# Kernel optimization log

Hardware: AMD Instinct MI355X
Metric: run time of the kernel (lower is better)

The kernel has to match this reference:

```python
import jax, jax.numpy as jnp
import numpy as np
import math

FACTOR = 5  # module default

def setup_inputs() -> dict:
    key = jax.random.key(0)
    kq, kk, kv, ki = jax.random.split(key, 4)
    B, L, S, H, D = 2, 4096, 4096, 8, 64
    u_part = min(FACTOR * math.ceil(math.log(L)), S)  # 45: sampled keys per query
    return {
        "queries": jax.random.normal(kq, (B, L, H, D), jnp.float32),
        "keys": jax.random.normal(kk, (B, S, H, D), jnp.float32),
        "values": jax.random.normal(kv, (B, S, H, D), jnp.float32),
        "index_sample": jax.random.randint(ki, (L, u_part), 0, S),
    }

def reference(queries, keys, values, index_sample):
    # queries: [B,L,H,D], keys/values: [B,S,H,D], index_sample: [L,u_part]
    B, L, H, D = queries.shape
    S = keys.shape[1]
    Q = jnp.transpose(queries, (0, 2, 1, 3))  # [B,H,L,D]
    K = jnp.transpose(keys, (0, 2, 1, 3))     # [B,H,S,D]
    V = jnp.transpose(values, (0, 2, 1, 3))   # [B,H,S,D]
    U_part = min(FACTOR * math.ceil(math.log(S)), L)  # n_top queries (static)

    # --- _prob_QK: sample keys, sparsity measure M, top-k queries ---
    K_sample = K[:, :, index_sample, :]  # gather -> [B,H,L,u_part,D]
    QK_sample = jnp.einsum('bhld,bhlud->bhlu', Q, K_sample)  # [B,H,L,u_part]
    M = QK_sample.max(axis=-1) - QK_sample.sum(axis=-1) / S  # [B,H,L]
    _, M_top = jax.lax.top_k(M, U_part)                      # [B,H,U_part]
    Q_reduce = jnp.take_along_axis(Q, M_top[..., None], axis=2)  # [B,H,U_part,D]
    scores = jnp.einsum('bhud,bhsd->bhus', Q_reduce, K)          # [B,H,U_part,S]

    # --- mask_flag=False branch: plain scaled softmax attention ---
    scale = 1.0 / math.sqrt(D)
    attn = jax.nn.softmax(scores * scale, axis=-1)  # [B,H,U_part,S]
    context = jnp.einsum('bhus,bhsd->bhud', attn, V)  # [B,H,U_part,D]
    return context, attn
```

## Files before the change

kernel.cpp:

```cpp
#include <hip/hip_runtime.h>

#define BB 2
#define LL 4096
#define SS 4096
#define HH 8
#define DD 64
#define UU 45
#define SCALE 0.125f
#define NCH 32
#define CHK 128

__global__ __launch_bounds__(256) void k_compute_M(
    const float* __restrict__ q, const float* __restrict__ k,
    const int* __restrict__ idx, float* __restrict__ M) {
  __shared__ int sidx[16 * UU];
  int tid = threadIdx.x;
  int bh = blockIdx.x & 15;
  int l0 = (blockIdx.x >> 4) << 4;
  for (int i = tid; i < 16 * UU; i += 256) sidx[i] = idx[(long)l0 * UU + i];
  __syncthreads();

  int slot = tid >> 4;
  int sub  = tid & 15;
  int l = l0 + slot;
  int b = bh >> 3, h = bh & 7;

  const float4* qp = (const float4*)(q + (((long)b * LL + l) * HH + h) * DD);
  float4 qq = qp[sub];
  const float* kb = k + (long)b * SS * HH * DD + h * DD;

  float mx = -INFINITY, sm = 0.f;
  #pragma unroll 5
  for (int u = 0; u < UU; ++u) {
    int s = sidx[slot * UU + u];
    float4 kk4 = ((const float4*)(kb + (long)s * (HH * DD)))[sub];
    float p = qq.x * kk4.x + qq.y * kk4.y + qq.z * kk4.z + qq.w * kk4.w;
    #pragma unroll
    for (int off = 8; off; off >>= 1) p += __shfl_xor(p, off, 16);
    mx = fmaxf(mx, p);
    sm += p;
  }
  if (sub == 0) M[(long)bh * LL + l] = mx - sm * (1.0f / SS);
}

__global__ __launch_bounds__(256) void k_topk(
    const float* __restrict__ M, int* __restrict__ Mtop) {
  __shared__ unsigned keys[LL];
  __shared__ int hist[256];
  __shared__ int wsum[4];
  __shared__ int sh_bin, sh_gtwin;
  __shared__ int ccount, ecount;
  __shared__ unsigned cand_key[64];
  __shared__ int cand_idx[64];
  __shared__ int elist[LL];

  int bh = blockIdx.x, tid = threadIdx.x;
  int lane = tid & 63, w = tid >> 6;
  const float* m = M + (long)bh * LL;
  for (int i = tid; i < LL; i += 256) {
    union { float f; unsigned u; } cv; cv.f = m[i];
    keys[i] = (cv.u & 0x80000000u) ? ~cv.u : (cv.u | 0x80000000u);
  }
  if (tid == 0) { ccount = 0; ecount = 0; }
  __syncthreads();

  unsigned prefix = 0, pmask = 0;
  int need = UU, above = 0;

  for (int shift = 24; shift >= 0; shift -= 8) {
    hist[tid] = 0;
    __syncthreads();
    #pragma unroll
    for (int j = 0; j < 16; ++j) {
      unsigned kk = keys[tid + (j << 8)];
      if ((kk & pmask) == prefix) atomicAdd(&hist[(kk >> shift) & 255], 1);
    }
    __syncthreads();
    int v = hist[tid];
    int sfx = v;
    #pragma unroll
    for (int st = 1; st < 64; st <<= 1) {
      int o = __shfl_down(sfx, st, 64);
      if (lane + st < 64) sfx += o;
    }
    if (lane == 0) wsum[w] = sfx;
    __syncthreads();
    for (int t = w + 1; t < 4; ++t) sfx += wsum[t];
    int gt = sfx - v;
    if (gt < need && sfx >= need) {
      sh_bin = tid;
      sh_gtwin = gt;
    }
    __syncthreads();
    prefix |= ((unsigned)sh_bin << shift);
    pmask  |= (255u << shift);
    need  -= sh_gtwin;
    above += sh_gtwin;
    __syncthreads();
  }
  unsigned T = prefix;

  #pragma unroll
  for (int j = 0; j < 16; ++j) {
    int i = tid + (j << 8);
    unsigned kk = keys[i];
    if (kk > T)      { int p = atomicAdd(&ccount, 1); cand_key[p] = kk; cand_idx[p] = i; }
    else if (kk == T){ int p = atomicAdd(&ecount, 1); elist[p] = i; }
  }
  __syncthreads();
  int nc = ccount, ne = ecount;
  for (int t = tid; t < nc; t += 256) {
    unsigned kk = cand_key[t]; int ii = cand_idx[t]; int r = 0;
    for (int j = 0; j < nc; ++j)
      r += (cand_key[j] > kk) || (cand_key[j] == kk && cand_idx[j] < ii);
    Mtop[bh * UU + r] = ii;
  }
  for (int t = tid; t < ne; t += 256) {
    int ii = elist[t]; int r = 0;
    for (int j = 0; j < ne; ++j) r += (elist[j] < ii);
    if (r < need) Mtop[bh * UU + above + r] = ii;
  }
}

__global__ __launch_bounds__(256) void k_fused(
    const float* __restrict__ q, const float* __restrict__ k,
    const float* __restrict__ v, const int* __restrict__ Mtop,
    float* __restrict__ attn, float* __restrict__ part,
    float2* __restrict__ stats) {
  __shared__ float smem[4 * UU * DD];
  __shared__ float gm[UU], gl[UU];
  float* qr = smem;
  float* sp = smem + UU * DD;

  int ch = blockIdx.x, bh = blockIdx.y;
  int b = bh >> 3, h = bh & 7;
  int tid = threadIdx.x;
  int lane = tid & 63, w = tid >> 6;
  int s0 = ch * CHK;

  for (int i = tid; i < UU * DD; i += 256) {
    int u = i >> 6, d = i & 63;
    int l = Mtop[bh * UU + u];
    qr[i] = q[(((long)b * LL + l) * HH + h) * DD + d];
  }
  __syncthreads();

  {
    int sl = tid & 127, uh = tid >> 7;
    float4 kr[16];
    const float4* kp = (const float4*)(k + (((long)b * SS + s0 + sl) * HH + h) * DD);
    #pragma unroll
    for (int j = 0; j < 16; ++j) kr[j] = kp[j];
    int u0 = uh ? 23 : 0, u1 = uh ? UU : 23;
    for (int u = u0; u < u1; ++u) {
      const float4* qp = (const float4*)(qr + u * DD);
      float acc = 0.f;
      #pragma unroll
      for (int j = 0; j < 16; ++j) {
        float4 qq = qp[j];
        acc += qq.x * kr[j].x + qq.y * kr[j].y + qq.z * kr[j].z + qq.w * kr[j].w;
      }
      sp[sl * 52 + u] = acc * SCALE;
    }
  }
  __syncthreads();

  for (int u = w; u < UU; u += 4) {
    float a0 = sp[lane * 52 + u];
    float a1 = sp[(lane + 64) * 52 + u];
    float mx = fmaxf(a0, a1);
    #pragma unroll
    for (int off = 32; off; off >>= 1) mx = fmaxf(mx, __shfl_xor(mx, off, 64));
    if (lane == 0) gm[u] = mx;
  }
  __syncthreads();
  for (int i = tid; i < UU * CHK; i += 256) {
    int u = i >> 7, sl = i & 127;
    float p = __expf(sp[sl * 52 + u] - gm[u]);
    sp[sl * 52 + u] = p;
    attn[((long)bh * UU + u) * SS + s0 + sl] = p;
  }
  __syncthreads();
  for (int u = w; u < UU; u += 4) {
    float a0 = sp[lane * 52 + u];
    float a1 = sp[(lane + 64) * 52 + u];
    float e = a0 + a1;
    #pragma unroll
    for (int off = 32; off; off >>= 1) e += __shfl_xor(e, off, 64);
    if (lane == 0) gl[u] = e;
  }

  float acc[UU];
  #pragma unroll
  for (int u = 0; u < UU; ++u) acc[u] = 0.f;
  const float* vb = v + (long)b * SS * HH * DD + h * DD + lane;
  #pragma unroll 2
  for (int j = 0; j < 32; ++j) {
    int sl = (j << 2) + w;
    float vd = vb[(long)(s0 + sl) * (HH * DD)];
    const float* ar = sp + sl * 52;
    #pragma unroll
    for (int g = 0; g < 11; ++g) {
      float4 aa = *(const float4*)(ar + g * 4);
      acc[g * 4 + 0] += aa.x * vd;
      acc[g * 4 + 1] += aa.y * vd;
      acc[g * 4 + 2] += aa.z * vd;
      acc[g * 4 + 3] += aa.w * vd;
    }
    acc[44] += ar[44] * vd;
  }

  __syncthreads();
  #pragma unroll
  for (int u = 0; u < UU; ++u) smem[(w * UU + u) * DD + lane] = acc[u];
  __syncthreads();
  long base = ((long)bh * NCH + ch) * (UU * DD);
  for (int i = tid; i < UU * DD; i += 256)
    part[base + i] = smem[i] + smem[UU * DD + i] + smem[2 * UU * DD + i] + smem[3 * UU * DD + i];
  if (tid < UU)
    stats[((long)bh * UU + tid) * NCH + ch] = make_float2(gm[tid], gl[tid]);
}

__global__ __launch_bounds__(256) void k_epilogue(
    const float2* __restrict__ stats, const float* __restrict__ part,
    float* __restrict__ attn, float* __restrict__ ctx) {
  __shared__ float f[NCH];
  __shared__ float2 st_s[NCH];
  int bid = blockIdx.x, tid = threadIdx.x;
  if (bid < BB * HH * UU) {
    long row = bid;
    const float2* st = stats + row * NCH;
    if (tid < NCH) st_s[tid] = st[tid];
    __syncthreads();
    if (tid == 0) {
      float M = -INFINITY;
      #pragma unroll
      for (int c = 0; c < NCH; ++c) M = fmaxf(M, st_s[c].x);
      float L = 0.f;
      #pragma unroll
      for (int c = 0; c < NCH; ++c) L += st_s[c].y * __expf(st_s[c].x - M);
      float inv = 1.0f / L;
      #pragma unroll
      for (int c = 0; c < NCH; ++c) f[c] = __expf(st_s[c].x - M) * inv;
    }
    __syncthreads();
    float4* a = (float4*)(attn + row * SS);
    #pragma unroll
    for (int g = 0; g < 4; ++g) {
      int i4 = g * 256 + tid;
      float ff = f[i4 >> 5];
      float4 vv = a[i4];
      vv.x *= ff; vv.y *= ff; vv.z *= ff; vv.w *= ff;
      a[i4] = vv;
    }
  } else {
    int e = (bid - BB * HH * UU) * 256 + tid;
    int bh = e / (UU * DD);
    int r = e - bh * (UU * DD);
    int u = r >> 6;
    const float2* st = stats + ((long)bh * UU + u) * NCH;
    float M = -INFINITY;
    #pragma unroll
    for (int c = 0; c < NCH; ++c) M = fmaxf(M, st[c].x);
    float L = 0.f, s = 0.f;
    #pragma unroll
    for (int c = 0; c < NCH; ++c) {
      float ee = __expf(st[c].x - M);
      L += st[c].y * ee;
      s += part[((long)bh * NCH + c) * (UU * DD) + r] * ee;
    }
    ctx[e] = s / L;
  }
}

__global__ __launch_bounds__(256) void k_scores(
    const float* __restrict__ q, const float* __restrict__ k,
    const int* __restrict__ Mtop, float* __restrict__ attn) {
  __shared__ float qr[UU * DD];
  int bh = blockIdx.y;
  int b = bh >> 3, h = bh & 7;
  for (int i = threadIdx.x; i < UU * DD; i += 256) {
    int u = i >> 6, d = i & 63;
    int l = Mtop[bh * UU + u];
    qr[i] = q[(((long)b * LL + l) * HH + h) * DD + d];
  }
  __syncthreads();
  int s = blockIdx.x * 256 + threadIdx.x;
  float4 kr[16];
  const float4* kp = (const float4*)(k + (((long)b * SS + s) * HH + h) * DD);
  #pragma unroll
  for (int j = 0; j < 16; ++j) kr[j] = kp[j];
  for (int u = 0; u < UU; ++u) {
    const float4* qp = (const float4*)(qr + u * DD);
    float acc = 0.f;
    #pragma unroll
    for (int j = 0; j < 16; ++j) {
      float4 qq = qp[j];
      acc += qq.x * kr[j].x + qq.y * kr[j].y + qq.z * kr[j].z + qq.w * kr[j].w;
    }
    attn[((long)bh * UU + u) * SS + s] = acc * SCALE;
  }
}

__global__ __launch_bounds__(256) void k_softmax(float* __restrict__ attn) {
  __shared__ float red[256];
  long row = blockIdx.x;
  float* a = attn + row * SS;
  float v[16];
  float mx = -INFINITY;
  #pragma unroll
  for (int j = 0; j < 16; ++j) {
    v[j] = a[j * 256 + threadIdx.x];
    mx = fmaxf(mx, v[j]);
  }
  red[threadIdx.x] = mx;
  __syncthreads();
  for (int st = 128; st; st >>= 1) {
    if (threadIdx.x < st) red[threadIdx.x] = fmaxf(red[threadIdx.x], red[threadIdx.x + st]);
    __syncthreads();
  }
  mx = red[0];
  __syncthreads();
  float sm = 0.f;
  #pragma unroll
  for (int j = 0; j < 16; ++j) {
    v[j] = __expf(v[j] - mx);
    sm += v[j];
  }
  red[threadIdx.x] = sm;
  __syncthreads();
  for (int st = 128; st; st >>= 1) {
    if (threadIdx.x < st) red[threadIdx.x] += red[threadIdx.x + st];
    __syncthreads();
  }
  float inv = 1.0f / red[0];
  #pragma unroll
  for (int j = 0; j < 16; ++j) a[j * 256 + threadIdx.x] = v[j] * inv;
}

__global__ __launch_bounds__(256) void k_context_fb(
    const float* __restrict__ attn, const float* __restrict__ v,
    float* __restrict__ ctx) {
  __shared__ float red[4][DD];
  int row = blockIdx.x;
  int bh = row / UU;
  int b = bh >> 3, h = bh & 7;
  int lane = threadIdx.x & 63;
  int grp = threadIdx.x >> 6;
  const float* a = attn + (long)row * SS;
  float acc = 0.f;
  for (int s = grp; s < SS; s += 4)
    acc += a[s] * v[(((long)b * SS + s) * HH + h) * DD + lane];
  red[grp][lane] = acc;
  __syncthreads();
  if (grp == 0)
    ctx[(long)row * DD + lane] = red[0][lane] + red[1][lane] + red[2][lane] + red[3][lane];
}

extern "C" void kernel_launch(void* const* d_in, const int* in_sizes, int n_in,
                              void* d_out, int out_size, void* d_ws, size_t ws_size,
                              hipStream_t stream) {
  const float* q   = (const float*)d_in[0];
  const float* k   = (const float*)d_in[1];
  const float* v   = (const float*)d_in[2];
  const int*   idx = (const int*)d_in[3];

  float* out  = (float*)d_out;
  float* ctx  = out;
  float* attn = out + (long)BB * HH * UU * DD;

  float* M    = attn;
  int*   Mtop = (int*)ctx;

  k_compute_M<<<BB * HH * LL / 16, 256, 0, stream>>>(q, k, idx, M);
  k_topk<<<BB * HH, 256, 0, stream>>>(M, Mtop);

  size_t part_bytes  = (size_t)BB * HH * NCH * UU * DD * sizeof(float);
  size_t stats_bytes = (size_t)BB * HH * UU * NCH * sizeof(float2);
  if (ws_size >= part_bytes + stats_bytes) {
    float*  part  = (float*)d_ws;
    float2* stats = (float2*)((char*)d_ws + part_bytes);
    k_fused<<<dim3(NCH, BB * HH), 256, 0, stream>>>(q, k, v, Mtop, attn, part, stats);
    int nctx = (BB * HH * UU * DD) / 256;
    k_epilogue<<<BB * HH * UU + nctx, 256, 0, stream>>>(stats, part, attn, ctx);
  } else {
    k_scores<<<dim3(SS / 256, BB * HH), 256, 0, stream>>>(q, k, Mtop, attn);
    k_softmax<<<BB * HH * UU, 256, 0, stream>>>(attn);
    k_context_fb<<<BB * HH * UU, 256, 0, stream>>>(attn, v, ctx);
  }
}
```

Baseline: 108.6 us.

## Split fused attention kernel across two query-row halves per block

The fused scores/softmax/context kernel now uses a 3D grid that splits the 45 selected queries into two halves of 23 and 22, so each block handles half the rows. This doubles the block count from 512 to 1024 and cuts shared memory and accumulator registers per block, which should raise occupancy. The cross-wave reduction now runs serially through a small staging buffer instead of a 4x-wide shared array. In exchange, each K and V chunk is loaded twice, once per half, and the serialized reduction adds barriers.

```diff
diff --git a/kernel.cpp b/kernel.cpp
--- a/kernel.cpp
+++ b/kernel.cpp
@@ -9,6 +9,7 @@
 #define SCALE 0.125f
 #define NCH 32
 #define CHK 128
+#define SPP 28
 
 __global__ __launch_bounds__(256) void k_compute_M(
     const float* __restrict__ q, const float* __restrict__ k,
@@ -127,98 +128,108 @@
     const float* __restrict__ v, const int* __restrict__ Mtop,
     float* __restrict__ attn, float* __restrict__ part,
     float2* __restrict__ stats) {
-  __shared__ float smem[4 * UU * DD];
-  __shared__ float gm[UU], gl[UU];
-  float* qr = smem;
-  float* sp = smem + UU * DD;
-
-  int ch = blockIdx.x, bh = blockIdx.y;
+  __shared__ float qr[23 * DD];
+  __shared__ float sp[CHK * SPP];
+  __shared__ float gm[23], gl[23];
+
+  int ch = blockIdx.x, uh = blockIdx.y, bh = blockIdx.z;
   int b = bh >> 3, h = bh & 7;
+  int ubase = uh * 23;
+  int ucount = uh ? 22 : 23;
   int tid = threadIdx.x;
   int lane = tid & 63, w = tid >> 6;
   int s0 = ch * CHK;
 
-  for (int i = tid; i < UU * DD; i += 256) {
-    int u = i >> 6, d = i & 63;
-    int l = Mtop[bh * UU + u];
+  for (int i = tid; i < ucount * DD; i += 256) {
+    int uu = i >> 6, d = i & 63;
+    int l = Mtop[bh * UU + ubase + uu];
     qr[i] = q[(((long)b * LL + l) * HH + h) * DD + d];
   }
   __syncthreads();
 
   {
-    int sl = tid & 127, uh = tid >> 7;
+    int sl = tid & 127, ph = tid >> 7;
     float4 kr[16];
     const float4* kp = (const float4*)(k + (((long)b * SS + s0 + sl) * HH + h) * DD);
     #pragma unroll
     for (int j = 0; j < 16; ++j) kr[j] = kp[j];
-    int u0 = uh ? 23 : 0, u1 = uh ? UU : 23;
-    for (int u = u0; u < u1; ++u) {
-      const float4* qp = (const float4*)(qr + u * DD);
+    int mid = (ucount + 1) >> 1;
+    int u_lo = ph ? mid : 0, u_hi = ph ? ucount : mid;
+    for (int uu = u_lo; uu < u_hi; ++uu) {
+      const float4* qp = (const float4*)(qr + uu * DD);
       float acc = 0.f;
       #pragma unroll
       for (int j = 0; j < 16; ++j) {
         float4 qq = qp[j];
         acc += qq.x * kr[j].x + qq.y * kr[j].y + qq.z * kr[j].z + qq.w * kr[j].w;
       }
-      sp[sl * 52 + u] = acc * SCALE;
-    }
-  }
-  __syncthreads();
-
-  for (int u = w; u < UU; u += 4) {
-    float a0 = sp[lane * 52 + u];
-    float a1 = sp[(lane + 64) * 52 + u];
+      sp[sl * SPP + uu] = acc * SCALE;
+    }
+  }
+  __syncthreads();
+
+  for (int uu = w; uu < ucount; uu += 4) {
+    float a0 = sp[lane * SPP + uu];
+    float a1 = sp[(lane + 64) * SPP + uu];
     float mx = fmaxf(a0, a1);
     #pragma unroll
     for (int off = 32; off; off >>= 1) mx = fmaxf(mx, __shfl_xor(mx, off, 64));
-    if (lane == 0) gm[u] = mx;
-  }
-  __syncthreads();
-  for (int i = tid; i < UU * CHK; i += 256) {
-    int u = i >> 7, sl = i & 127;
-    float p = __expf(sp[sl * 52 + u] - gm[u]);
-    sp[sl * 52 + u] = p;
-    attn[((long)bh * UU + u) * SS + s0 + sl] = p;
-  }
-  __syncthreads();
-  for (int u = w; u < UU; u += 4) {
-    float a0 = sp[lane * 52 + u];
-    float a1 = sp[(lane + 64) * 52 + u];
+    if (lane == 0) gm[uu] = mx;
+  }
+  __syncthreads();
+  for (int i = tid; i < ucount * CHK; i += 256) {
+    int uu = i >> 7, sl = i & 127;
+    float p = __expf(sp[sl * SPP + uu] - gm[uu]);
+    sp[sl * SPP + uu] = p;
+    attn[((long)bh * UU + ubase + uu) * SS + s0 + sl] = p;
+  }
+  __syncthreads();
+  for (int uu = w; uu < ucount; uu += 4) {
+    float a0 = sp[lane * SPP + uu];
+    float a1 = sp[(lane + 64) * SPP + uu];
     float e = a0 + a1;
     #pragma unroll
     for (int off = 32; off; off >>= 1) e += __shfl_xor(e, off, 64);
-    if (lane == 0) gl[u] = e;
-  }
-
-  float acc[UU];
-  #pragma unroll
-  for (int u = 0; u < UU; ++u) acc[u] = 0.f;
+    if (lane == 0) gl[uu] = e;
+  }
+
+  float acc[23];
+  #pragma unroll
+  for (int uu = 0; uu < 23; ++uu) acc[uu] = 0.f;
   const float* vb = v + (long)b * SS * HH * DD + h * DD + lane;
   #pragma unroll 2
   for (int j = 0; j < 32; ++j) {
     int sl = (j << 2) + w;
     float vd = vb[(long)(s0 + sl) * (HH * DD)];
-    const float* ar = sp + sl * 52;
-    #pragma unroll
-    for (int g = 0; g < 11; ++g) {
+    const float* ar = sp + sl * SPP;
+    #pragma unroll
+    for (int g = 0; g < 5; ++g) {
       float4 aa = *(const float4*)(ar + g * 4);
       acc[g * 4 + 0] += aa.x * vd;
       acc[g * 4 + 1] += aa.y * vd;
       acc[g * 4 + 2] += aa.z * vd;
       acc[g * 4 + 3] += aa.w * vd;
     }
-    acc[44] += ar[44] * vd;
-  }
-
-  __syncthreads();
-  #pragma unroll
-  for (int u = 0; u < UU; ++u) smem[(w * UU + u) * DD + lane] = acc[u];
-  __syncthreads();
-  long base = ((long)bh * NCH + ch) * (UU * DD);
-  for (int i = tid; i < UU * DD; i += 256)
-    part[base + i] = smem[i] + smem[UU * DD + i] + smem[2 * UU * DD + i] + smem[3 * UU * DD + i];
-  if (tid < UU)
-    stats[((long)bh * UU + tid) * NCH + ch] = make_float2(gm[tid], gl[tid]);
+    acc[20] += ar[20] * vd;
+    acc[21] += ar[21] * vd;
+    if (ucount == 23) acc[22] += ar[22] * vd;
+  }
+
+  __syncthreads();
+  float* stg = qr;
+  if (w == 0) { for (int uu = 0; uu < ucount; ++uu) stg[uu * DD + lane] = acc[uu]; }
+  __syncthreads();
+  if (w == 1) { for (int uu = 0; uu < ucount; ++uu) stg[uu * DD + lane] += acc[uu]; }
+  __syncthreads();
+  if (w == 2) { for (int uu = 0; uu < ucount; ++uu) stg[uu * DD + lane] += acc[uu]; }
+  __syncthreads();
+  if (w == 3) { for (int uu = 0; uu < ucount; ++uu) stg[uu * DD + lane] += acc[uu]; }
+  __syncthreads();
+
+  long base = ((long)bh * NCH + ch) * (UU * DD) + (long)ubase * DD;
+  for (int i = tid; i < ucount * DD; i += 256) part[base + i] = stg[i];
+  if (tid < ucount)
+    stats[((long)bh * UU + ubase + tid) * NCH + ch] = make_float2(gm[tid], gl[tid]);
 }
 
 __global__ __launch_bounds__(256) void k_epilogue(
@@ -380,7 +391,7 @@
   if (ws_size >= part_bytes + stats_bytes) {
     float*  part  = (float*)d_ws;
     float2* stats = (float2*)((char*)d_ws + part_bytes);
-    k_fused<<<dim3(NCH, BB * HH), 256, 0, stream>>>(q, k, v, Mtop, attn, part, stats);
+    k_fused<<<dim3(NCH, 2, BB * HH), 256, 0, stream>>>(q, k, v, Mtop, attn, part, stats);
     int nctx = (BB * HH * UU * DD) / 256;
     k_epilogue<<<BB * HH * UU + nctx, 256, 0, stream>>>(stats, part, attn, ctx);
   } else {
```

Measured after the change: 128.6 us. 18.5% more time.

## Template fused attention on chunk count, use 64 chunks and per-wave row split

Applied to the files above, without the earlier changes.

The fused score/softmax/context kernel becomes a template on the number of key chunks, and the launch picks 64 chunks of 64 keys when the workspace is large enough, which doubles the block count to 1024. The context accumulation now splits the 45 query rows across the four waves (12 rows each) instead of having each wave keep all 45 accumulators over a strided subset of keys. This removes the cross-wave shared-memory reduction and reduces register pressure. The cost is more partial buffers and stats for the epilogue to combine, and a larger workspace requirement.

```diff
diff --git a/kernel.cpp b/kernel.cpp
--- a/kernel.cpp
+++ b/kernel.cpp
@@ -7,8 +7,7 @@
 #define DD 64
 #define UU 45
 #define SCALE 0.125f
-#define NCH 32
-#define CHK 128
+#define SPP 52
 
 __global__ __launch_bounds__(256) void k_compute_M(
     const float* __restrict__ q, const float* __restrict__ k,
@@ -122,15 +121,17 @@
   }
 }
 
-__global__ __launch_bounds__(256) void k_fused(
+template <int NCHV>
+__global__ __launch_bounds__(256) void k_fused_t(
     const float* __restrict__ q, const float* __restrict__ k,
     const float* __restrict__ v, const int* __restrict__ Mtop,
     float* __restrict__ attn, float* __restrict__ part,
     float2* __restrict__ stats) {
-  __shared__ float smem[4 * UU * DD];
-  __shared__ float gm[UU], gl[UU];
-  float* qr = smem;
-  float* sp = smem + UU * DD;
+  constexpr int CHK = SS / NCHV;
+  constexpr int PH  = 256 / CHK;
+  __shared__ float qr[UU * DD];
+  __shared__ float sp[CHK * SPP];
+  __shared__ float gm[48], gl[48];
 
   int ch = blockIdx.x, bh = blockIdx.y;
   int b = bh >> 3, h = bh & 7;
@@ -139,116 +140,127 @@
   int s0 = ch * CHK;
 
   for (int i = tid; i < UU * DD; i += 256) {
-    int u = i >> 6, d = i & 63;
-    int l = Mtop[bh * UU + u];
+    int uu = i >> 6, d = i & 63;
+    int l = Mtop[bh * UU + uu];
     qr[i] = q[(((long)b * LL + l) * HH + h) * DD + d];
   }
   __syncthreads();
 
   {
-    int sl = tid & 127, uh = tid >> 7;
+    int sl = tid & (CHK - 1), ph = tid / CHK;
     float4 kr[16];
     const float4* kp = (const float4*)(k + (((long)b * SS + s0 + sl) * HH + h) * DD);
     #pragma unroll
     for (int j = 0; j < 16; ++j) kr[j] = kp[j];
-    int u0 = uh ? 23 : 0, u1 = uh ? UU : 23;
-    for (int u = u0; u < u1; ++u) {
-      const float4* qp = (const float4*)(qr + u * DD);
+    for (int uu = ph; uu < UU; uu += PH) {
+      const float4* qp = (const float4*)(qr + uu * DD);
       float acc = 0.f;
       #pragma unroll
       for (int j = 0; j < 16; ++j) {
         float4 qq = qp[j];
         acc += qq.x * kr[j].x + qq.y * kr[j].y + qq.z * kr[j].z + qq.w * kr[j].w;
       }
-      sp[sl * 52 + u] = acc * SCALE;
-    }
-  }
-  __syncthreads();
-
-  for (int u = w; u < UU; u += 4) {
-    float a0 = sp[lane * 52 + u];
-    float a1 = sp[(lane + 64) * 52 + u];
-    float mx = fmaxf(a0, a1);
+      sp[sl * SPP + uu] = acc * SCALE;
+    }
+  }
+  __syncthreads();
+
+  for (int uu = w; uu < UU; uu += 4) {
+    float mx;
+    if constexpr (CHK == 64) {
+      mx = sp[lane * SPP + uu];
+    } else {
+      mx = fmaxf(sp[lane * SPP + uu], sp[(lane + 64) * SPP + uu]);
+    }
     #pragma unroll
     for (int off = 32; off; off >>= 1) mx = fmaxf(mx, __shfl_xor(mx, off, 64));
-    if (lane == 0) gm[u] = mx;
-  }
-  __syncthreads();
+    if (lane == 0) gm[uu] = mx;
+  }
+  __syncthreads();
+
   for (int i = tid; i < UU * CHK; i += 256) {
-    int u = i >> 7, sl = i & 127;
-    float p = __expf(sp[sl * 52 + u] - gm[u]);
-    sp[sl * 52 + u] = p;
-    attn[((long)bh * UU + u) * SS + s0 + sl] = p;
-  }
-  __syncthreads();
-  for (int u = w; u < UU; u += 4) {
-    float a0 = sp[lane * 52 + u];
-    float a1 = sp[(lane + 64) * 52 + u];
-    float e = a0 + a1;
+    int uu = i / CHK, sl = i & (CHK - 1);
+    float p = __expf(sp[sl * SPP + uu] - gm[uu]);
+    sp[sl * SPP + uu] = p;
+    attn[((long)bh * UU + uu) * SS + s0 + sl] = p;
+  }
+  __syncthreads();
+
+  for (int uu = w; uu < UU; uu += 4) {
+    float e;
+    if constexpr (CHK == 64) {
+      e = sp[lane * SPP + uu];
+    } else {
+      e = sp[lane * SPP + uu] + sp[(lane + 64) * SPP + uu];
+    }
     #pragma unroll
     for (int off = 32; off; off >>= 1) e += __shfl_xor(e, off, 64);
-    if (lane == 0) gl[u] = e;
-  }
-
-  float acc[UU];
-  #pragma unroll
-  for (int u = 0; u < UU; ++u) acc[u] = 0.f;
+    if (lane == 0) gl[uu] = e;
+  }
+
+  int ur = w * 12;
+  float acc[12];
+  #pragma unroll
+  for (int j = 0; j < 12; ++j) acc[j] = 0.f;
   const float* vb = v + (long)b * SS * HH * DD + h * DD + lane;
-  #pragma unroll 2
-  for (int j = 0; j < 32; ++j) {
-    int sl = (j << 2) + w;
+  #pragma unroll 4
+  for (int sl = 0; sl < CHK; ++sl) {
     float vd = vb[(long)(s0 + sl) * (HH * DD)];
-    const float* ar = sp + sl * 52;
-    #pragma unroll
-    for (int g = 0; g < 11; ++g) {
-      float4 aa = *(const float4*)(ar + g * 4);
-      acc[g * 4 + 0] += aa.x * vd;
-      acc[g * 4 + 1] += aa.y * vd;
-      acc[g * 4 + 2] += aa.z * vd;
-      acc[g * 4 + 3] += aa.w * vd;
-    }
-    acc[44] += ar[44] * vd;
-  }
-
-  __syncthreads();
-  #pragma unroll
-  for (int u = 0; u < UU; ++u) smem[(w * UU + u) * DD + lane] = acc[u];
-  __syncthreads();
-  long base = ((long)bh * NCH + ch) * (UU * DD);
-  for (int i = tid; i < UU * DD; i += 256)
-    part[base + i] = smem[i] + smem[UU * DD + i] + smem[2 * UU * DD + i] + smem[3 * UU * DD + i];
+    const float* ar = sp + sl * SPP + ur;
+    float4 a0 = *(const float4*)(ar);
+    float4 a1 = *(const float4*)(ar + 4);
+    acc[0] += a0.x * vd; acc[1] += a0.y * vd;
+    acc[2] += a0.z * vd; acc[3] += a0.w * vd;
+    acc[4] += a1.x * vd; acc[5] += a1.y * vd;
+    acc[6] += a1.z * vd; acc[7] += a1.w * vd;
+    if (w == 3) {
+      acc[8] += ar[8] * vd;
+    } else {
+      float4 a2 = *(const float4*)(ar + 8);
+      acc[8]  += a2.x * vd; acc[9]  += a2.y * vd;
+      acc[10] += a2.z * vd; acc[11] += a2.w * vd;
+    }
+  }
+  int un = (w == 3) ? 9 : 12;
+  long pbase = ((long)bh * NCHV + ch) * (UU * DD);
+  for (int j = 0; j < un; ++j)
+    part[pbase + (ur + j) * DD + lane] = acc[j];
+
+  __syncthreads();
   if (tid < UU)
-    stats[((long)bh * UU + tid) * NCH + ch] = make_float2(gm[tid], gl[tid]);
-}
-
-__global__ __launch_bounds__(256) void k_epilogue(
+    stats[((long)bh * UU + tid) * NCHV + ch] = make_float2(gm[tid], gl[tid]);
+}
+
+template <int NCHV>
+__global__ __launch_bounds__(256) void k_epilogue_t(
     const float2* __restrict__ stats, const float* __restrict__ part,
     float* __restrict__ attn, float* __restrict__ ctx) {
-  __shared__ float f[NCH];
-  __shared__ float2 st_s[NCH];
+  constexpr int CPF4 = (SS / NCHV) / 4;
+  __shared__ float f[NCHV];
+  __shared__ float2 st_s[NCHV];
+  __shared__ float ML[2];
   int bid = blockIdx.x, tid = threadIdx.x;
   if (bid < BB * HH * UU) {
-    long row = bid;
-    const float2* st = stats + row * NCH;
-    if (tid < NCH) st_s[tid] = st[tid];
+    const float2* st = stats + (long)bid * NCHV;
+    if (tid < NCHV) st_s[tid] = st[tid];
     __syncthreads();
     if (tid == 0) {
       float M = -INFINITY;
       #pragma unroll
-      for (int c = 0; c < NCH; ++c) M = fmaxf(M, st_s[c].x);
+      for (int c = 0; c < NCHV; ++c) M = fmaxf(M, st_s[c].x);
       float L = 0.f;
       #pragma unroll
-      for (int c = 0; c < NCH; ++c) L += st_s[c].y * __expf(st_s[c].x - M);
-      float inv = 1.0f / L;
-      #pragma unroll
-      for (int c = 0; c < NCH; ++c) f[c] = __expf(st_s[c].x - M) * inv;
-    }
-    __syncthreads();
-    float4* a = (float4*)(attn + row * SS);
+      for (int c = 0; c < NCHV; ++c) L += st_s[c].y * __expf(st_s[c].x - M);
+      ML[0] = M; ML[1] = 1.0f / L;
+    }
+    __syncthreads();
+    if (tid < NCHV) f[tid] = __expf(st_s[tid].x - ML[0]) * ML[1];
+    __syncthreads();
+    float4* a = (float4*)(attn + (long)bid * SS);
     #pragma unroll
     for (int g = 0; g < 4; ++g) {
       int i4 = g * 256 + tid;
-      float ff = f[i4 >> 5];
+      float ff = f[i4 / CPF4];
       float4 vv = a[i4];
       vv.x *= ff; vv.y *= ff; vv.z *= ff; vv.w *= ff;
       a[i4] = vv;
@@ -258,16 +270,15 @@
     int bh = e / (UU * DD);
     int r = e - bh * (UU * DD);
     int u = r >> 6;
-    const float2* st = stats + ((long)bh * UU + u) * NCH;
+    const float2* st = stats + ((long)bh * UU + u) * NCHV;
     float M = -INFINITY;
     #pragma unroll
-    for (int c = 0; c < NCH; ++c) M = fmaxf(M, st[c].x);
+    for (int c = 0; c < NCHV; ++c) M = fmaxf(M, st[c].x);
     float L = 0.f, s = 0.f;
-    #pragma unroll
-    for (int c = 0; c < NCH; ++c) {
+    for (int c = 0; c < NCHV; ++c) {
       float ee = __expf(st[c].x - M);
       L += st[c].y * ee;
-      s += part[((long)bh * NCH + c) * (UU * DD) + r] * ee;
+      s += part[((long)bh * NCHV + c) * (UU * DD) + r] * ee;
     }
     ctx[e] = s / L;
   }
@@ -375,14 +386,20 @@
   k_compute_M<<<BB * HH * LL / 16, 256, 0, stream>>>(q, k, idx, M);
   k_topk<<<BB * HH, 256, 0, stream>>>(M, Mtop);
 
-  size_t part_bytes  = (size_t)BB * HH * NCH * UU * DD * sizeof(float);
-  size_t stats_bytes = (size_t)BB * HH * UU * NCH * sizeof(float2);
-  if (ws_size >= part_bytes + stats_bytes) {
+  const size_t pd = (size_t)BB * HH * UU * DD * sizeof(float);
+  const size_t sd = (size_t)BB * HH * UU * sizeof(float2);
+  int nctx = (BB * HH * UU * DD) / 256;
+
+  if (ws_size >= 64 * (pd + sd)) {
     float*  part  = (float*)d_ws;
-    float2* stats = (float2*)((char*)d_ws + part_bytes);
-    k_fused<<<dim3(NCH, BB * HH), 256, 0, stream>>>(q, k, v, Mtop, attn, part, stats);
-    int nctx = (BB * HH * UU * DD) / 256;
-    k_epilogue<<<BB * HH * UU + nctx, 256, 0, stream>>>(stats, part, attn, ctx);
+    float2* stats = (float2*)((char*)d_ws + 64 * pd);
+    k_fused_t<64><<<dim3(64, BB * HH), 256, 0, stream>>>(q, k, v, Mtop, attn, part, stats);
+    k_epilogue_t<64><<<BB * HH * UU + nctx, 256, 0, stream>>>(stats, part, attn, ctx);
+  } else if (ws_size >= 32 * (pd + sd)) {
+    float*  part  = (float*)d_ws;
+    float2* stats = (float2*)((char*)d_ws + 32 * pd);
+    k_fused_t<32><<<dim3(32, BB * HH), 256, 0, stream>>>(q, k, v, Mtop, attn, part, stats);
+    k_epilogue_t<32><<<BB * HH * UU + nctx, 256, 0, stream>>>(stats, part, attn, ctx);
   } else {
     k_scores<<<dim3(SS / 256, BB * HH), 256, 0, stream>>>(q, k, Mtop, attn);
     k_softmax<<<BB * HH * UU, 256, 0, stream>>>(attn);
```

Result: slower. 128.7 us (+18.5%).
